# Performance work log

Hardware: AMD Instinct MI355X
Metric: run time of the kernel (lower is better)

## Reference

```python
import jax, jax.numpy as jnp
import numpy as np

N_NODES = 100000
N_EDGES = 3200000
N_GRAPHS = 1024
F_IN = 78
H = 128
BN_EPS = 1e-5


def setup_inputs() -> dict:
    key = jax.random.key(0)
    ks = jax.random.split(key, 10)
    x = jax.random.normal(ks[0], (N_NODES, F_IN), dtype=jnp.float32)
    edge_index = jax.random.randint(ks[1], (2, N_EDGES), 0, N_NODES, dtype=jnp.int64)
    batch = jnp.sort(jax.random.randint(ks[2], (N_NODES,), 0, N_GRAPHS, dtype=jnp.int64))
    s_in = 1.0 / np.sqrt(F_IN)
    s_h = 1.0 / np.sqrt(H)
    return {
        "x": x,
        "edge_index": edge_index,
        "batch": batch,
        "W1_0": jax.random.normal(ks[3], (F_IN, H), dtype=jnp.float32) * s_in,
        "b1_0": jnp.zeros((H,), jnp.float32),
        "W2_0": jax.random.normal(ks[4], (H, H), dtype=jnp.float32) * s_h,
        "b2_0": jnp.zeros((H,), jnp.float32),
        "W1": jax.random.normal(ks[5], (4, H, H), dtype=jnp.float32) * s_h,
        "b1": jnp.zeros((4, H), jnp.float32),
        "W2": jax.random.normal(ks[6], (4, H, H), dtype=jnp.float32) * s_h,
        "b2": jnp.zeros((4, H), jnp.float32),
        "gamma": jnp.ones((5, H), jnp.float32),
        "beta": jnp.zeros((5, H), jnp.float32),
        "Wf": jax.random.normal(ks[7], (2 * H, H), dtype=jnp.float32) * (1.0 / np.sqrt(2 * H)),
        "bf": jnp.zeros((H,), jnp.float32),
    }


def _gin_layer(x, src, dst, W1l, b1l, W2l, b2l, g, bta):
    # GINConv, eps=0: h_i = x_i + sum_{(j->i) in E} x_j, then 2-layer MLP
    agg = jax.ops.segment_sum(x[src], dst, num_segments=N_NODES)  # [N, F]
    h = x + agg
    h = jax.nn.relu(h @ W1l + b1l) @ W2l + b2l
    h = jax.nn.relu(h)
    # BatchNorm1d (training mode: biased batch statistics)
    mu = jnp.mean(h, axis=0)
    var = jnp.mean(jnp.square(h - mu), axis=0)
    return (h - mu) * (g / jnp.sqrt(var + BN_EPS)) + bta


def reference(x, edge_index, batch, W1_0, b1_0, W2_0, b2_0, W1, b1, W2, b2, gamma, beta, Wf, bf):
    src, dst = edge_index[0], edge_index[1]
    # layer 0 (no residual: dims 78 -> 128)
    h = _gin_layer(x, src, dst, W1_0, b1_0, W2_0, b2_0, gamma[0], beta[0])
    # layers 1..4 with residual
    for i in range(4):
        h_new = _gin_layer(h, src, dst, W1[i], b1[i], W2[i], b2[i], gamma[i + 1], beta[i + 1])
        h = h + h_new
    # global mean pool
    sums = jax.ops.segment_sum(h, batch, num_segments=N_GRAPHS)  # [G, H]
    counts = jax.ops.segment_sum(jnp.ones((h.shape[0],), h.dtype), batch, num_segments=N_GRAPHS)
    mean_pool = sums / jnp.maximum(counts, 1.0)[:, None]
    # global max pool (empty segments -> 0)
    max_pool = jax.ops.segment_max(h, batch, num_segments=N_GRAPHS)
    max_pool = jnp.where(counts[:, None] > 0, max_pool, 0.0)
    combined = jnp.concatenate([mean_pool, max_pool], axis=1)  # [G, 2H]
    return combined @ Wf + bf
```

## Files before the change

kernel.cpp:

```cpp
#include <hip/hip_runtime.h>
#include <float.h>

#define N_NODES 100000
#define N_EDGES 3200000
#define N_GRAPHS 1024
#define F_IN 78
#define H 128
#define BN_EPS 1e-5f

#define BK_SHIFT 7
#define BK_NODES 128
#define NBUCKETS ((N_NODES + BK_NODES - 1) / BK_NODES)

#define P3_BLOCKS 200
#define P3_CHUNK 16000

using short8 = __attribute__((ext_vector_type(8))) short;
using f32x4v = __attribute__((ext_vector_type(4))) float;

__device__ __forceinline__ unsigned short f2bf(float f) {
    unsigned int u = __float_as_uint(f);
    unsigned int r = (u + 0x7fffu + ((u >> 16) & 1u)) >> 16;
    return (unsigned short)r;
}
__device__ __forceinline__ float bf_lo(unsigned int u) { return __uint_as_float(u << 16); }
__device__ __forceinline__ float bf_hi(unsigned int u) { return __uint_as_float(u & 0xffff0000u); }
__device__ __forceinline__ float bf1(unsigned short u) { return __uint_as_float((unsigned int)u << 16); }


__global__ __launch_bounds__(256) void k_hist(const int* __restrict__ dst,
                                              int* __restrict__ bofs) {
    __shared__ int lcnt[NBUCKETS];
    for (int i = threadIdx.x; i < NBUCKETS; i += 256) lcnt[i] = 0;
    __syncthreads();
    int base = blockIdx.x * P3_CHUNK;
    for (int j = threadIdx.x; j < P3_CHUNK; j += 256)
        atomicAdd(&lcnt[dst[base + j] >> BK_SHIFT], 1);
    __syncthreads();
    for (int i = threadIdx.x; i < NBUCKETS; i += 256)
        bofs[blockIdx.x * NBUCKETS + i] = lcnt[i];
}

__global__ __launch_bounds__(256) void k_scan_a(int* __restrict__ bofs,
                                                int* __restrict__ btot) {
    __shared__ int part[256];
    int b = blockIdx.x, t = threadIdx.x;
    int val = (t < P3_BLOCKS) ? bofs[t * NBUCKETS + b] : 0;
    part[t] = val;
    __syncthreads();
    if (t == 0) {
        int run = 0;
        for (int u = 0; u < P3_BLOCKS; ++u) { int tmp = part[u]; part[u] = run; run += tmp; }
        btot[b] = run;
    }
    __syncthreads();
    if (t < P3_BLOCKS) bofs[t * NBUCKETS + b] = part[t];
}

__global__ __launch_bounds__(1024) void k_scan_b(const int* __restrict__ btot,
                                                 int* __restrict__ bbase,
                                                 int* __restrict__ row_start) {
    __shared__ int tot[1024];
    int t = threadIdx.x;
    tot[t] = (t < NBUCKETS) ? btot[t] : 0;
    __syncthreads();
    if (t == 0) {
        int acc = 0;
        for (int i = 0; i < NBUCKETS; ++i) { int v = tot[i]; tot[i] = acc; acc += v; }
    }
    __syncthreads();
    if (t < NBUCKETS) bbase[t] = tot[t];
    if (t == 0) {
        bbase[NBUCKETS] = N_EDGES;
        row_start[N_NODES] = N_EDGES;
    }
}

__global__ __launch_bounds__(256) void k_p3b(const int* __restrict__ src,
                                             const int* __restrict__ dst,
                                             const int* __restrict__ bofs,
                                             const int* __restrict__ bbase,
                                             unsigned int* __restrict__ ebuf) {
    __shared__ int cur[NBUCKETS];
    for (int i = threadIdx.x; i < NBUCKETS; i += 256)
        cur[i] = bbase[i] + bofs[blockIdx.x * NBUCKETS + i];
    __syncthreads();
    int base = blockIdx.x * P3_CHUNK;
    for (int j = threadIdx.x; j < P3_CHUNK; j += 256) {
        int d = dst[base + j];
        int p = atomicAdd(&cur[d >> BK_SHIFT], 1);
        ebuf[p] = ((unsigned int)src[base + j] << 7) | (unsigned int)(d & (BK_NODES - 1));
    }
}

__global__ __launch_bounds__(256) void k_p4(const int* __restrict__ bbase,
                                            const unsigned int* __restrict__ ebuf,
                                            int* __restrict__ esrc,
                                            int* __restrict__ row_start) {
    __shared__ int cur[BK_NODES];
    __shared__ int start[BK_NODES];
    int b = blockIdx.x;
    int nodeBase = b << BK_SHIFT;
    int nLocal = min(BK_NODES, N_NODES - nodeBase);
    if (threadIdx.x < BK_NODES) cur[threadIdx.x] = 0;
    __syncthreads();
    int s = bbase[b], e = bbase[b + 1];
    for (int p = s + threadIdx.x; p < e; p += 256)
        atomicAdd(&cur[ebuf[p] & (BK_NODES - 1)], 1);
    __syncthreads();
    if (threadIdx.x == 0) {
        int run = s;
        for (int i = 0; i < nLocal; ++i) { start[i] = run; run += cur[i]; }
    }
    __syncthreads();
    if (threadIdx.x < nLocal) {
        row_start[nodeBase + threadIdx.x] = start[threadIdx.x];
        cur[threadIdx.x] = start[threadIdx.x];
    }
    __syncthreads();
    for (int p = s + threadIdx.x; p < e; p += 256) {
        unsigned int ed = ebuf[p];
        int q = atomicAdd(&cur[ed & (BK_NODES - 1)], 1);
        esrc[q] = (int)(ed >> 7);
    }
}


__global__ void k_cast_x(const float* __restrict__ x, unsigned short* __restrict__ xb) {
    int i = blockIdx.x * blockDim.x + threadIdx.x;
    if (i >= N_NODES * 96) return;
    int node = i / 96;
    int c = i - node * 96;
    float v = (c < F_IN) ? x[(size_t)node * F_IN + c] : 0.f;
    xb[i] = f2bf(v);
}

__global__ void k_cast_w(const float* __restrict__ W2_0, const float* __restrict__ W1,
                         const float* __restrict__ W2, unsigned short* __restrict__ Wt) {
    int i = blockIdx.x * blockDim.x + threadIdx.x;
    if (i >= 9 * H * H) return;
    int w = i >> 14, r = i & 16383;
    int n = r >> 7, k = r & 127;
    const float* s = (w == 0) ? W2_0 : (w <= 4 ? W1 + (w - 1) * H * H : W2 + (w - 5) * H * H);
    Wt[i] = f2bf(s[k * H + n]);
}

__global__ void k_cast_w0(const float* __restrict__ W1_0, unsigned short* __restrict__ Wt0) {
    int i = blockIdx.x * blockDim.x + threadIdx.x;
    if (i >= H * 96) return;
    int n = i / 96, k = i - n * 96;
    Wt0[i] = f2bf((k < F_IN) ? W1_0[k * H + n] : 0.f);
}


__global__ void k_gather96(const unsigned int* __restrict__ xw,
                           const int* __restrict__ row_start, const int* __restrict__ esrc,
                           unsigned int* __restrict__ out) {
    int wave = threadIdx.x >> 6;
    int lane = threadIdx.x & 63;
    int node = blockIdx.x * 4 + wave;
    int s = row_start[node], e = row_start[node + 1];
    bool act = lane < 48;
    unsigned int su = act ? xw[node * 48 + lane] : 0u;
    float aA[8], aB[8];
#pragma unroll
    for (int j = 0; j < 8; ++j) { aA[j] = 0.f; aB[j] = 0.f; }
    aA[0] = bf_lo(su); aB[0] = bf_hi(su);
    int p = s;
    for (; p + 16 <= e; p += 16) {
        int idx[16];
#pragma unroll
        for (int j = 0; j < 16; ++j) idx[j] = esrc[p + j];
        unsigned int u[16];
#pragma unroll
        for (int j = 0; j < 16; ++j) u[j] = act ? xw[idx[j] * 48 + lane] : 0u;
#pragma unroll
        for (int j = 0; j < 16; ++j) { aA[j & 7] += bf_lo(u[j]); aB[j & 7] += bf_hi(u[j]); }
    }
    for (; p + 4 <= e; p += 4) {
        int i0 = esrc[p], i1 = esrc[p + 1], i2 = esrc[p + 2], i3 = esrc[p + 3];
        unsigned int u0 = act ? xw[i0 * 48 + lane] : 0u;
        unsigned int u1 = act ? xw[i1 * 48 + lane] : 0u;
        unsigned int u2 = act ? xw[i2 * 48 + lane] : 0u;
        unsigned int u3 = act ? xw[i3 * 48 + lane] : 0u;
        aA[0] += bf_lo(u0); aB[0] += bf_hi(u0); aA[1] += bf_lo(u1); aB[1] += bf_hi(u1);
        aA[2] += bf_lo(u2); aB[2] += bf_hi(u2); aA[3] += bf_lo(u3); aB[3] += bf_hi(u3);
    }
    for (; p < e; ++p) {
        unsigned int u = act ? xw[esrc[p] * 48 + lane] : 0u;
        aA[0] += bf_lo(u); aB[0] += bf_hi(u);
    }
    if (act) {
        float rx = ((aA[0] + aA[1]) + (aA[2] + aA[3])) + ((aA[4] + aA[5]) + (aA[6] + aA[7]));
        float ry = ((aB[0] + aB[1]) + (aB[2] + aB[3])) + ((aB[4] + aB[5]) + (aB[6] + aB[7]));
        out[node * 48 + lane] = (unsigned int)f2bf(rx) | ((unsigned int)f2bf(ry) << 16);
    }
}

__global__ void k_gather128b(const unsigned int* __restrict__ hw,
                             const int* __restrict__ row_start, const int* __restrict__ esrc,
                             unsigned int* __restrict__ aggb) {
    int wave = threadIdx.x >> 6;
    int lane = threadIdx.x & 63;
    int node = blockIdx.x * 4 + wave;
    int s = row_start[node], e = row_start[node + 1];
    unsigned int su = hw[node * 64 + lane];
    float aA[8], aB[8];
#pragma unroll
    for (int j = 0; j < 8; ++j) { aA[j] = 0.f; aB[j] = 0.f; }
    aA[0] = bf_lo(su); aB[0] = bf_hi(su);
    int p = s;
    for (; p + 16 <= e; p += 16) {
        int idx[16];
#pragma unroll
        for (int j = 0; j < 16; ++j) idx[j] = esrc[p + j];
        unsigned int u[16];
#pragma unroll
        for (int j = 0; j < 16; ++j) u[j] = hw[idx[j] * 64 + lane];
#pragma unroll
        for (int j = 0; j < 16; ++j) { aA[j & 7] += bf_lo(u[j]); aB[j & 7] += bf_hi(u[j]); }
    }
    for (; p + 4 <= e; p += 4) {
        int i0 = esrc[p], i1 = esrc[p + 1], i2 = esrc[p + 2], i3 = esrc[p + 3];
        unsigned int u0 = hw[i0 * 64 + lane];
        unsigned int u1 = hw[i1 * 64 + lane];
        unsigned int u2 = hw[i2 * 64 + lane];
        unsigned int u3 = hw[i3 * 64 + lane];
        aA[0] += bf_lo(u0); aB[0] += bf_hi(u0); aA[1] += bf_lo(u1); aB[1] += bf_hi(u1);
        aA[2] += bf_lo(u2); aB[2] += bf_hi(u2); aA[3] += bf_lo(u3); aB[3] += bf_hi(u3);
    }
    for (; p < e; ++p) {
        unsigned int u = hw[esrc[p] * 64 + lane];
        aA[0] += bf_lo(u); aB[0] += bf_hi(u);
    }
    float rx = ((aA[0] + aA[1]) + (aA[2] + aA[3])) + ((aA[4] + aA[5]) + (aA[6] + aA[7]));
    float ry = ((aB[0] + aB[1]) + (aB[2] + aB[3])) + ((aB[4] + aB[5]) + (aB[6] + aB[7]));
    aggb[node * 64 + lane] = (unsigned int)f2bf(rx) | ((unsigned int)f2bf(ry) << 16);
}


template <int NK1>
__global__ __launch_bounds__(256) void k_mlp(const short* __restrict__ A,
                                             const short* __restrict__ Wt1,
                                             const float* __restrict__ b1v,
                                             const short* __restrict__ Wt2,
                                             const float* __restrict__ b2v,
                                             unsigned short* __restrict__ out,
                                             float* __restrict__ gsum,
                                             float* __restrict__ gss) {
    const int K1 = NK1 * 32;
    __shared__ unsigned short act1[64 * H];
    __shared__ float lsum[H], lss[H];
    if (threadIdx.x < H) { lsum[threadIdx.x] = 0.f; lss[threadIdx.x] = 0.f; }
    int wave = threadIdx.x >> 6, lane = threadIdx.x & 63;
    int r0 = blockIdx.x * 64 + wave * 16;
    int lm = lane & 15, lk = lane >> 4;
    int arow = r0 + lm;
    if (arow >= N_NODES) arow = N_NODES - 1;
    const short8* Arow = (const short8*)(A + (size_t)arow * K1);
    f32x4v acc[8];
#pragma unroll
    for (int n = 0; n < 8; ++n) {
        float bv = b1v[n * 16 + lm];
        acc[n] = (f32x4v){bv, bv, bv, bv};
    }
#pragma unroll
    for (int ks = 0; ks < NK1; ++ks) {
        short8 af = Arow[ks * 4 + lk];
#pragma unroll
        for (int n = 0; n < 8; ++n) {
            const short8* Brow = (const short8*)(Wt1 + (size_t)(n * 16 + lm) * K1);
            short8 bfr = Brow[ks * 4 + lk];
            acc[n] = __builtin_amdgcn_mfma_f32_16x16x32_bf16(af, bfr, acc[n], 0, 0, 0);
        }
    }
#pragma unroll
    for (int n = 0; n < 8; ++n) {
        int colb = (n * 16 + lm) * 2;
#pragma unroll
        for (int rg = 0; rg < 4; ++rg) {
            int rl = wave * 16 + lk * 4 + rg;
            int byte = (rl * 256 + colb) ^ ((rl & 7) << 4);
            *(unsigned short*)((char*)act1 + byte) = f2bf(fmaxf(acc[n][rg], 0.f));
        }
    }
    __syncthreads();
    f32x4v acc2[8];
#pragma unroll
    for (int n = 0; n < 8; ++n) {
        float bv = b2v[n * 16 + lm];
        acc2[n] = (f32x4v){bv, bv, bv, bv};
    }
    int rlr = wave * 16 + lm;
#pragma unroll
    for (int ks = 0; ks < 4; ++ks) {
        int byte = (rlr * 256 + ks * 64 + lk * 16) ^ ((rlr & 7) << 4);
        short8 af = *(const short8*)((char*)act1 + byte);
#pragma unroll
        for (int n = 0; n < 8; ++n) {
            const short8* Brow = (const short8*)(Wt2 + (size_t)(n * 16 + lm) * H);
            short8 bfr = Brow[ks * 4 + lk];
            acc2[n] = __builtin_amdgcn_mfma_f32_16x16x32_bf16(af, bfr, acc2[n], 0, 0, 0);
        }
    }
#pragma unroll
    for (int n = 0; n < 8; ++n) {
        int col = n * 16 + lm;
        float s = 0.f, q = 0.f;
#pragma unroll
        for (int rg = 0; rg < 4; ++rg) {
            int r = r0 + lk * 4 + rg;
            if (r < N_NODES) {
                float v = fmaxf(acc2[n][rg], 0.f);
                out[(size_t)r * H + col] = f2bf(v);
                s += v;
                q += v * v;
            }
        }
        atomicAdd(&lsum[col], s);
        atomicAdd(&lss[col], q);
    }
    __syncthreads();
    if (threadIdx.x < H) {
        atomicAdd(&gsum[threadIdx.x], lsum[threadIdx.x]);
        atomicAdd(&gss[threadIdx.x], lss[threadIdx.x]);
    }
}


__global__ void k_bnfinal(float* __restrict__ gsum, float* __restrict__ gss,
                          const float* __restrict__ gamma, const float* __restrict__ beta,
                          float* __restrict__ scale, float* __restrict__ shift) {
    int c = threadIdx.x;
    const float inv_n = 1.f / (float)N_NODES;
    float sv = gsum[c], qv = gss[c];
    gsum[c] = 0.f;
    gss[c] = 0.f;
    float mu = sv * inv_n;
    float var = fmaxf(qv * inv_n - mu * mu, 0.f);
    float sc = gamma[c] * rsqrtf(var + BN_EPS);
    scale[c] = sc;
    shift[c] = beta[c] - mu * sc;
}

template <bool RES>
__global__ void k_bnapply(const uint2* __restrict__ vb, const float* __restrict__ scale,
                          const float* __restrict__ shift, uint2* __restrict__ hb) {
    int idx = blockIdx.x * blockDim.x + threadIdx.x;
    if (idx >= N_NODES * H / 4) return;
    int c4 = idx & 31;
    uint2 pv = vb[idx];
    float4 val = make_float4(bf_lo(pv.x), bf_hi(pv.x), bf_lo(pv.y), bf_hi(pv.y));
    float4 sc = reinterpret_cast<const float4*>(scale)[c4];
    float4 sh = reinterpret_cast<const float4*>(shift)[c4];
    float4 r;
    r.x = val.x * sc.x + sh.x;
    r.y = val.y * sc.y + sh.y;
    r.z = val.z * sc.z + sh.z;
    r.w = val.w * sc.w + sh.w;
    if (RES) {
        uint2 hv = hb[idx];
        r.x += bf_lo(hv.x); r.y += bf_hi(hv.x); r.z += bf_lo(hv.y); r.w += bf_hi(hv.y);
    }
    uint2 pk;
    pk.x = (unsigned int)f2bf(r.x) | ((unsigned int)f2bf(r.y) << 16);
    pk.y = (unsigned int)f2bf(r.z) | ((unsigned int)f2bf(r.w) << 16);
    hb[idx] = pk;
}


__global__ void k_bounds(const int* __restrict__ batch, int* __restrict__ row_begin) {
    int i = blockIdx.x * blockDim.x + threadIdx.x;
    if (i >= N_NODES) return;
    int bi = batch[i];
    int bp = (i == 0) ? -1 : batch[i - 1];
    for (int g = bp + 1; g <= bi; ++g) row_begin[g] = i;
    if (i == N_NODES - 1) {
        for (int g = bi + 1; g <= N_GRAPHS; ++g) row_begin[g] = N_NODES;
    }
}

__global__ void k_pool_f(const unsigned short* __restrict__ act, const float* __restrict__ scale,
                         const float* __restrict__ shift, const unsigned short* __restrict__ hb3,
                         const int* __restrict__ row_begin, float* __restrict__ pooled) {
    int g = blockIdx.x;
    int c = threadIdx.x;
    float sc = scale[c], sh = shift[c];
    int s = row_begin[g], e = row_begin[g + 1];
    float sum = 0.f, mx = -FLT_MAX;
    for (int i = s; i < e; ++i) {
        float v = bf1(hb3[(size_t)i * H + c]) + sc * bf1(act[(size_t)i * H + c]) + sh;
        sum += v;
        mx = fmaxf(mx, v);
    }
    int cnt = e - s;
    pooled[g * 256 + c]       = (cnt > 0) ? sum / (float)cnt : 0.f;
    pooled[g * 256 + 128 + c] = (cnt > 0) ? mx : 0.f;
}

__global__ void k_final(const float* __restrict__ pooled, const float* __restrict__ Wf,
                        const float* __restrict__ bf, float* __restrict__ out) {
    __shared__ float ps[256];
    int g = blockIdx.x, c = threadIdx.x;
    ps[c] = pooled[g * 256 + c];
    ps[128 + c] = pooled[g * 256 + 128 + c];
    __syncthreads();
    float acc = bf[c];
#pragma unroll 8
    for (int k = 0; k < 256; ++k) acc += ps[k] * Wf[k * H + c];
    out[g * H + c] = acc;
}


extern "C" void kernel_launch(void* const* d_in, const int* in_sizes, int n_in,
                              void* d_out, int out_size, void* d_ws, size_t ws_size,
                              hipStream_t stream) {
    const float* x     = (const float*)d_in[0];
    const int*   ei    = (const int*)d_in[1];
    const int*   src   = ei;
    const int*   dst   = ei + N_EDGES;
    const int*   batch = (const int*)d_in[2];
    const float* W1_0  = (const float*)d_in[3];
    const float* b1_0  = (const float*)d_in[4];
    const float* W2_0  = (const float*)d_in[5];
    const float* b2_0  = (const float*)d_in[6];
    const float* W1    = (const float*)d_in[7];
    const float* b1    = (const float*)d_in[8];
    const float* W2    = (const float*)d_in[9];
    const float* b2    = (const float*)d_in[10];
    const float* gamma = (const float*)d_in[11];
    const float* beta  = (const float*)d_in[12];
    const float* Wf    = (const float*)d_in[13];
    const float* bf    = (const float*)d_in[14];
    float* out = (float*)d_out;

    char* ws = (char*)d_ws;
    size_t off = 0;
    auto alloc = [&](size_t bytes) -> void* {
        void* p = ws + off;
        off = (off + bytes + 255) & ~(size_t)255;
        return p;
    };

    uint2* hb   = (uint2*)alloc((size_t)N_NODES * H * 2);
    unsigned int*   aggb  = (unsigned int*)alloc((size_t)N_NODES * H * 2);
    unsigned short* act2b = (unsigned short*)alloc((size_t)N_NODES * H * 2);
    unsigned short* xb    = (unsigned short*)alloc((size_t)N_NODES * 96 * 2);
    unsigned int*   agg0b = (unsigned int*)alloc((size_t)N_NODES * 48 * 4);
    unsigned short* Wtall = (unsigned short*)alloc((size_t)9 * H * H * 2);
    unsigned short* Wt0   = (unsigned short*)alloc((size_t)H * 96 * 2);
    int* row_start = (int*)alloc((size_t)(N_NODES + 1) * 4);
    int* esrc      = (int*)alloc((size_t)N_EDGES * 4);
    unsigned int* ebuf = (unsigned int*)alloc((size_t)N_EDGES * 4);
    int* bofs      = (int*)alloc((size_t)P3_BLOCKS * NBUCKETS * 4);
    int* btot      = (int*)alloc((size_t)NBUCKETS * 4);
    int* bbase     = (int*)alloc((size_t)(NBUCKETS + 1) * 4);
    float* gsum  = (float*)alloc(H * 4);
    float* gss   = (float*)alloc(H * 4);
    float* scale = (float*)alloc(H * 4);
    float* shift = (float*)alloc(H * 4);
    int* row_begin = (int*)alloc((size_t)(N_GRAPHS + 1) * 4);
    float* pooled  = (float*)alloc((size_t)N_GRAPHS * 256 * 4);

    k_cast_x<<<(N_NODES * 96 + 255) / 256, 256, 0, stream>>>(x, xb);
    k_cast_w<<<(9 * H * H + 255) / 256, 256, 0, stream>>>(W2_0, W1, W2, Wtall);
    k_cast_w0<<<(H * 96 + 255) / 256, 256, 0, stream>>>(W1_0, Wt0);

    k_hist<<<P3_BLOCKS, 256, 0, stream>>>(dst, bofs);
    k_scan_a<<<NBUCKETS, 256, 0, stream>>>(bofs, btot);
    k_scan_b<<<1, 1024, 0, stream>>>(btot, bbase, row_start);
    k_p3b<<<P3_BLOCKS, 256, 0, stream>>>(src, dst, bofs, bbase, ebuf);
    k_p4<<<NBUCKETS, 256, 0, stream>>>(bbase, ebuf, esrc, row_start);

    hipMemsetAsync(gsum, 0, H * 4, stream);
    hipMemsetAsync(gss, 0, H * 4, stream);

    const int mfma_grid = (N_NODES + 63) / 64;

    k_gather96<<<N_NODES / 4, 256, 0, stream>>>((const unsigned int*)xb, row_start, esrc, agg0b);
    k_mlp<3><<<mfma_grid, 256, 0, stream>>>((const short*)agg0b, (const short*)Wt0, b1_0,
                                            (const short*)Wtall, b2_0, act2b, gsum, gss);
    k_bnfinal<<<1, 128, 0, stream>>>(gsum, gss, gamma, beta, scale, shift);
    k_bnapply<false><<<N_NODES * H / 4 / 256, 256, 0, stream>>>((const uint2*)act2b,
                                                                scale, shift, hb);

    for (int l = 0; l < 4; ++l) {
        k_gather128b<<<N_NODES / 4, 256, 0, stream>>>((const unsigned int*)hb, row_start,
                                                      esrc, aggb);
        k_mlp<4><<<mfma_grid, 256, 0, stream>>>((const short*)aggb,
                                                (const short*)(Wtall + (1 + l) * H * H),
                                                b1 + l * H,
                                                (const short*)(Wtall + (5 + l) * H * H),
                                                b2 + l * H, act2b, gsum, gss);
        k_bnfinal<<<1, 128, 0, stream>>>(gsum, gss, gamma + (l + 1) * H, beta + (l + 1) * H,
                                         scale, shift);
        if (l < 3) {
            k_bnapply<true><<<N_NODES * H / 4 / 256, 256, 0, stream>>>((const uint2*)act2b,
                                                                       scale, shift, hb);
        }
    }

    k_bounds<<<(N_NODES + 255) / 256, 256, 0, stream>>>(batch, row_begin);
    k_pool_f<<<N_GRAPHS, 128, 0, stream>>>(act2b, scale, shift,
                                           (const unsigned short*)hb, row_begin, pooled);
    k_final<<<N_GRAPHS, 128, 0, stream>>>(pooled, Wf, bf, out);
}
```

Measured before the change: 1.241 ms.

## Store hidden features in column-sliced layout for cache-friendly edge gathers

Hidden state h is stored as 8 column slices of 16 bf16 channels each, laid out [slice][node][16]. The gather kernel launches one block per (slice, node group), so each pass over the edges touches only a 3.2 MB slice, which is meant to keep gather traffic inside L2/LLC. Within a wave, 8 edges are handled in parallel, each by 8 lanes, and the partial sums are combined with shuffles. The MLP, bnapply and pooling kernels are changed to index the sliced layout. In exchange, the edge indices are read 8 times and each gather now loads only 32 bytes per row.

```diff
diff --git a/kernel.cpp b/kernel.cpp
--- a/kernel.cpp
+++ b/kernel.cpp
@@ -197,49 +197,52 @@
     }
 }
 
-__global__ void k_gather128b(const unsigned int* __restrict__ hw,
-                             const int* __restrict__ row_start, const int* __restrict__ esrc,
-                             unsigned int* __restrict__ aggb) {
+__global__ void k_gather_s(const unsigned int* __restrict__ hbs,
+                           const int* __restrict__ row_start, const int* __restrict__ esrc,
+                           unsigned int* __restrict__ aggs) {
     int wave = threadIdx.x >> 6;
     int lane = threadIdx.x & 63;
-    int node = blockIdx.x * 4 + wave;
+    int slice = blockIdx.x & 7;
+    int node = (blockIdx.x >> 3) * 4 + wave;
+    int c = lane & 7, eoff = lane >> 3;
+    const unsigned int* __restrict__ base = hbs + (size_t)slice * N_NODES * 8;
     int s = row_start[node], e = row_start[node + 1];
-    unsigned int su = hw[node * 64 + lane];
-    float aA[8], aB[8];
-#pragma unroll
-    for (int j = 0; j < 8; ++j) { aA[j] = 0.f; aB[j] = 0.f; }
-    aA[0] = bf_lo(su); aB[0] = bf_hi(su);
+    float a0 = 0.f, b0 = 0.f, a1 = 0.f, b1 = 0.f;
     int p = s;
     for (; p + 16 <= e; p += 16) {
-        int idx[16];
-#pragma unroll
-        for (int j = 0; j < 16; ++j) idx[j] = esrc[p + j];
-        unsigned int u[16];
-#pragma unroll
-        for (int j = 0; j < 16; ++j) u[j] = hw[idx[j] * 64 + lane];
-#pragma unroll
-        for (int j = 0; j < 16; ++j) { aA[j & 7] += bf_lo(u[j]); aB[j & 7] += bf_hi(u[j]); }
-    }
-    for (; p + 4 <= e; p += 4) {
-        int i0 = esrc[p], i1 = esrc[p + 1], i2 = esrc[p + 2], i3 = esrc[p + 3];
-        unsigned int u0 = hw[i0 * 64 + lane];
-        unsigned int u1 = hw[i1 * 64 + lane];
-        unsigned int u2 = hw[i2 * 64 + lane];
-        unsigned int u3 = hw[i3 * 64 + lane];
-        aA[0] += bf_lo(u0); aB[0] += bf_hi(u0); aA[1] += bf_lo(u1); aB[1] += bf_hi(u1);
-        aA[2] += bf_lo(u2); aB[2] += bf_hi(u2); aA[3] += bf_lo(u3); aB[3] += bf_hi(u3);
-    }
-    for (; p < e; ++p) {
-        unsigned int u = hw[esrc[p] * 64 + lane];
-        aA[0] += bf_lo(u); aB[0] += bf_hi(u);
-    }
-    float rx = ((aA[0] + aA[1]) + (aA[2] + aA[3])) + ((aA[4] + aA[5]) + (aA[6] + aA[7]));
-    float ry = ((aB[0] + aB[1]) + (aB[2] + aB[3])) + ((aB[4] + aB[5]) + (aB[6] + aB[7]));
-    aggb[node * 64 + lane] = (unsigned int)f2bf(rx) | ((unsigned int)f2bf(ry) << 16);
-}
-
-
-template <int NK1>
+        int i0 = esrc[p + eoff];
+        int i1 = esrc[p + 8 + eoff];
+        unsigned int u0 = base[(size_t)i0 * 8 + c];
+        unsigned int u1 = base[(size_t)i1 * 8 + c];
+        a0 += bf_lo(u0); b0 += bf_hi(u0);
+        a1 += bf_lo(u1); b1 += bf_hi(u1);
+    }
+    if (p + 8 <= e) {
+        int i0 = esrc[p + eoff];
+        unsigned int u0 = base[(size_t)i0 * 8 + c];
+        a0 += bf_lo(u0); b0 += bf_hi(u0);
+        p += 8;
+    }
+    if (p + eoff < e) {
+        int i0 = esrc[p + eoff];
+        unsigned int u0 = base[(size_t)i0 * 8 + c];
+        a1 += bf_lo(u0); b1 += bf_hi(u0);
+    }
+    float ax = a0 + a1, bx = b0 + b1;
+    ax += __shfl_xor(ax, 8);  bx += __shfl_xor(bx, 8);
+    ax += __shfl_xor(ax, 16); bx += __shfl_xor(bx, 16);
+    ax += __shfl_xor(ax, 32); bx += __shfl_xor(bx, 32);
+    if (eoff == 0) {
+        unsigned int su = base[(size_t)node * 8 + c];
+        float rx = bf_lo(su) + ax;
+        float ry = bf_hi(su) + bx;
+        aggs[(size_t)slice * N_NODES * 8 + (size_t)node * 8 + c] =
+            (unsigned int)f2bf(rx) | ((unsigned int)f2bf(ry) << 16);
+    }
+}
+
+
+template <int NK1, bool SLICED>
 __global__ __launch_bounds__(256) void k_mlp(const short* __restrict__ A,
                                              const short* __restrict__ Wt1,
                                              const float* __restrict__ b1v,
@@ -266,7 +269,13 @@
     }
 #pragma unroll
     for (int ks = 0; ks < NK1; ++ks) {
-        short8 af = Arow[ks * 4 + lk];
+        short8 af;
+        if constexpr (SLICED) {
+            int sl = 2 * ks + (lk >> 1);
+            af = *(const short8*)(A + ((size_t)sl * N_NODES + arow) * 16 + (lk & 1) * 8);
+        } else {
+            af = Arow[ks * 4 + lk];
+        }
 #pragma unroll
         for (int n = 0; n < 8; ++n) {
             const short8* Brow = (const short8*)(Wt1 + (size_t)(n * 16 + lm) * K1);
@@ -345,10 +354,12 @@
 
 template <bool RES>
 __global__ void k_bnapply(const uint2* __restrict__ vb, const float* __restrict__ scale,
-                          const float* __restrict__ shift, uint2* __restrict__ hb) {
+                          const float* __restrict__ shift, uint2* __restrict__ hbs) {
     int idx = blockIdx.x * blockDim.x + threadIdx.x;
     if (idx >= N_NODES * H / 4) return;
     int c4 = idx & 31;
+    int node = idx >> 5;
+    size_t hidx = ((size_t)(c4 >> 2) * N_NODES + node) * 4 + (c4 & 3);
     uint2 pv = vb[idx];
     float4 val = make_float4(bf_lo(pv.x), bf_hi(pv.x), bf_lo(pv.y), bf_hi(pv.y));
     float4 sc = reinterpret_cast<const float4*>(scale)[c4];
@@ -359,13 +370,13 @@
     r.z = val.z * sc.z + sh.z;
     r.w = val.w * sc.w + sh.w;
     if (RES) {
-        uint2 hv = hb[idx];
+        uint2 hv = hbs[hidx];
         r.x += bf_lo(hv.x); r.y += bf_hi(hv.x); r.z += bf_lo(hv.y); r.w += bf_hi(hv.y);
     }
     uint2 pk;
     pk.x = (unsigned int)f2bf(r.x) | ((unsigned int)f2bf(r.y) << 16);
     pk.y = (unsigned int)f2bf(r.z) | ((unsigned int)f2bf(r.w) << 16);
-    hb[idx] = pk;
+    hbs[hidx] = pk;
 }
 
 
@@ -381,15 +392,19 @@
 }
 
 __global__ void k_pool_f(const unsigned short* __restrict__ act, const float* __restrict__ scale,
-                         const float* __restrict__ shift, const unsigned short* __restrict__ hb3,
+                         const float* __restrict__ shift, const unsigned int* __restrict__ hbs,
                          const int* __restrict__ row_begin, float* __restrict__ pooled) {
     int g = blockIdx.x;
     int c = threadIdx.x;
     float sc = scale[c], sh = shift[c];
+    size_t sbase = (size_t)(c >> 4) * N_NODES * 8 + ((c >> 1) & 7);
+    int odd = c & 1;
     int s = row_begin[g], e = row_begin[g + 1];
     float sum = 0.f, mx = -FLT_MAX;
     for (int i = s; i < e; ++i) {
-        float v = bf1(hb3[(size_t)i * H + c]) + sc * bf1(act[(size_t)i * H + c]) + sh;
+        unsigned int u = hbs[sbase + (size_t)i * 8];
+        float hv = odd ? bf_hi(u) : bf_lo(u);
+        float v = hv + sc * bf1(act[(size_t)i * H + c]) + sh;
         sum += v;
         mx = fmaxf(mx, v);
     }
@@ -442,8 +457,8 @@
         return p;
     };
 
-    uint2* hb   = (uint2*)alloc((size_t)N_NODES * H * 2);
-    unsigned int*   aggb  = (unsigned int*)alloc((size_t)N_NODES * H * 2);
+    uint2* hbs  = (uint2*)alloc((size_t)N_NODES * H * 2);
+    unsigned int*   aggs  = (unsigned int*)alloc((size_t)N_NODES * H * 2);
     unsigned short* act2b = (unsigned short*)alloc((size_t)N_NODES * H * 2);
     unsigned short* xb    = (unsigned short*)alloc((size_t)N_NODES * 96 * 2);
     unsigned int*   agg0b = (unsigned int*)alloc((size_t)N_NODES * 48 * 4);
@@ -476,32 +491,33 @@
     hipMemsetAsync(gss, 0, H * 4, stream);
 
     const int mfma_grid = (N_NODES + 63) / 64;
+    const int slice_grid = (N_NODES / 4) * 8;
 
     k_gather96<<<N_NODES / 4, 256, 0, stream>>>((const unsigned int*)xb, row_start, esrc, agg0b);
-    k_mlp<3><<<mfma_grid, 256, 0, stream>>>((const short*)agg0b, (const short*)Wt0, b1_0,
-                                            (const short*)Wtall, b2_0, act2b, gsum, gss);
+    k_mlp<3, false><<<mfma_grid, 256, 0, stream>>>((const short*)agg0b, (const short*)Wt0, b1_0,
+                                                   (const short*)Wtall, b2_0, act2b, gsum, gss);
     k_bnfinal<<<1, 128, 0, stream>>>(gsum, gss, gamma, beta, scale, shift);
     k_bnapply<false><<<N_NODES * H / 4 / 256, 256, 0, stream>>>((const uint2*)act2b,
-                                                                scale, shift, hb);
+                                                                scale, shift, hbs);
 
     for (int l = 0; l < 4; ++l) {
-        k_gather128b<<<N_NODES / 4, 256, 0, stream>>>((const unsigned int*)hb, row_start,
-                                                      esrc, aggb);
-        k_mlp<4><<<mfma_grid, 256, 0, stream>>>((const short*)aggb,
-                                                (const short*)(Wtall + (1 + l) * H * H),
-                                                b1 + l * H,
-                                                (const short*)(Wtall + (5 + l) * H * H),
-                                                b2 + l * H, act2b, gsum, gss);
+        k_gather_s<<<slice_grid, 256, 0, stream>>>((const unsigned int*)hbs, row_start,
+                                                   esrc, aggs);
+        k_mlp<4, true><<<mfma_grid, 256, 0, stream>>>((const short*)aggs,
+                                                      (const short*)(Wtall + (1 + l) * H * H),
+                                                      b1 + l * H,
+                                                      (const short*)(Wtall + (5 + l) * H * H),
+                                                      b2 + l * H, act2b, gsum, gss);
         k_bnfinal<<<1, 128, 0, stream>>>(gsum, gss, gamma + (l + 1) * H, beta + (l + 1) * H,
                                          scale, shift);
         if (l < 3) {
             k_bnapply<true><<<N_NODES * H / 4 / 256, 256, 0, stream>>>((const uint2*)act2b,
-                                                                       scale, shift, hb);
+                                                                       scale, shift, hbs);
         }
     }
 
     k_bounds<<<(N_NODES + 255) / 256, 256, 0, stream>>>(batch, row_begin);
     k_pool_f<<<N_GRAPHS, 128, 0, stream>>>(act2b, scale, shift,
-                                           (const unsigned short*)hb, row_begin, pooled);
+                                           (const unsigned int*)hbs, row_begin, pooled);
     k_final<<<N_GRAPHS, 128, 0, stream>>>(pooled, Wf, bf, out);
 }
```

Measured after the change: 1.764 ms. 1.42x slower.
